# Kernel optimization log

Hardware: AMD Instinct MI355X
Metric: run time of the kernel (lower is better)

The kernel has to match this reference:

```python
import jax, jax.numpy as jnp
import numpy as np

N, IN_C, E = 50000, 512, 800000
H, C = 2, 64          # heads, per-head channels
HC = H * C            # 128
OUT_C = 2
B = 64                # number of graphs
EPS = 1e-5
NEG_SLOPE = 0.2


def gat_conv(x, src, dst, W, a_src, a_dst, bias):
    """PyG GATConv (concat=True, add_self_loops already included in src/dst)."""
    n = x.shape[0]
    h = (x @ W).reshape(n, H, C)                      # [N,H,C]
    alpha_src = (h * a_src[None]).sum(-1)             # [N,H]
    alpha_dst = (h * a_dst[None]).sum(-1)             # [N,H]
    e = jax.nn.leaky_relu(alpha_src[src] + alpha_dst[dst], NEG_SLOPE)  # [E,H]
    # segment softmax over incoming edges of each destination node
    m = jax.ops.segment_max(e, dst, num_segments=n)   # [N,H]
    ex = jnp.exp(e - m[dst])
    denom = jax.ops.segment_sum(ex, dst, num_segments=n)
    alpha = ex / denom[dst]                           # [E,H]
    msg = h[src] * alpha[:, :, None]                  # [E,H,C]
    out = jax.ops.segment_sum(msg, dst, num_segments=n)  # [N,H,C]
    return out.reshape(n, HC) + bias


def batch_norm(x, gamma, beta):
    # BatchNorm1d in training mode: batch statistics over the node dim
    mu = x.mean(0)
    var = x.var(0)
    return gamma * (x - mu) * jax.lax.rsqrt(var + EPS) + beta


def setup_inputs() -> dict:
    key = jax.random.key(0)
    ks = jax.random.split(key, 16)
    x = jax.random.normal(ks[0], (N, IN_C), dtype=jnp.float32)
    edge_index = jax.random.randint(ks[1], (2, E), 0, N, dtype=jnp.int64)
    batch = jnp.sort(jax.random.randint(ks[2], (N,), 0, B, dtype=jnp.int64))
    g = lambda k, sh, fan: jax.random.normal(k, sh, dtype=jnp.float32) * (1.0 / np.sqrt(fan))
    return {
        "x": x, "edge_index": edge_index, "batch": batch,
        "W1": g(ks[3], (IN_C, HC), IN_C),
        "att_src1": g(ks[4], (H, C), C), "att_dst1": g(ks[5], (H, C), C),
        "b1": jnp.zeros((HC,), jnp.float32),
        "gamma1": jnp.ones((HC,), jnp.float32), "beta1": jnp.zeros((HC,), jnp.float32),
        "W2": g(ks[6], (HC, HC), HC),
        "att_src2": g(ks[7], (H, C), C), "att_dst2": g(ks[8], (H, C), C),
        "b2": jnp.zeros((HC,), jnp.float32),
        "gamma2": jnp.ones((HC,), jnp.float32), "beta2": jnp.zeros((HC,), jnp.float32),
        "Wlin": g(ks[9], (HC, OUT_C), HC),
        "blin": jnp.zeros((OUT_C,), jnp.float32),
    }


def reference(x, edge_index, batch, W1, att_src1, att_dst1, b1, gamma1, beta1,
              W2, att_src2, att_dst2, b2, gamma2, beta2, Wlin, blin):
    n = x.shape[0]
    # GATConv adds self-loops by default
    loop = jnp.arange(n, dtype=edge_index.dtype)
    src = jnp.concatenate([edge_index[0], loop])
    dst = jnp.concatenate([edge_index[1], loop])

    h = gat_conv(x, src, dst, W1, att_src1, att_dst1, b1)
    h = jax.nn.relu(batch_norm(h, gamma1, beta1))
    h = gat_conv(h, src, dst, W2, att_src2, att_dst2, b2)
    h = jax.nn.relu(batch_norm(h, gamma2, beta2))

    # global mean pool over graphs
    sums = jax.ops.segment_sum(h, batch, num_segments=B)           # [B,HC]
    cnt = jax.ops.segment_sum(jnp.ones((n,), h.dtype), batch, num_segments=B)
    pooled = sums / jnp.maximum(cnt, 1.0)[:, None]
    return pooled @ Wlin + blin                                    # [B,OUT_C]
```

## Files before the change

### kernel.cpp

```cpp
#include <hip/hip_runtime.h>
#include <hip/hip_bf16.h>
#include <cstdint>
#include <cstddef>

#define NN      50000
#define IN_C    512
#define EE      800000
#define ETOT    850000
#define HH      2
#define CC      64
#define HC      128
#define BB      64
#define OUTC    2
#define NEG_SLOPE 0.2f
#define BN_EPS  1e-5f

#define NBLK_SCAN ((NN + 255) / 256)

typedef __bf16 bf16x8 __attribute__((ext_vector_type(8)));
typedef float  f32x4  __attribute__((ext_vector_type(4)));

__device__ __forceinline__ unsigned f2bf(float f) {
    __bf16 b = (__bf16)f;
    return (unsigned)__builtin_bit_cast(unsigned short, b);
}

__device__ __forceinline__ void edge_sd(const int* __restrict__ ei, int e, int& s, int& d) {
    if (e < EE) { s = ei[e]; d = ei[EE + e]; }
    else        { s = e - EE; d = e - EE; }
}

__global__ __launch_bounds__(256) void deg_kernel(const int* __restrict__ ei, int* __restrict__ deg)
{
    int e = blockIdx.x * 256 + threadIdx.x;
    if (e >= ETOT) return;
    int d = (e < EE) ? ei[EE + e] : (e - EE);
    atomicAdd(&deg[d], 1);
}

__global__ __launch_bounds__(256) void bsum_kernel(const int* __restrict__ deg, int* __restrict__ bsum)
{
    int i = blockIdx.x * 256 + threadIdx.x;
    int v = (i < NN) ? deg[i] : 0;
    int lane = threadIdx.x & 63, wv = threadIdx.x >> 6;
#pragma unroll
    for (int o = 32; o > 0; o >>= 1) v += __shfl_down(v, o);
    __shared__ int ws[4];
    if (lane == 0) ws[wv] = v;
    __syncthreads();
    if (threadIdx.x == 0) bsum[blockIdx.x] = ws[0] + ws[1] + ws[2] + ws[3];
}

__global__ __launch_bounds__(256) void bscan_kernel(
    const int* __restrict__ bsum, int* __restrict__ bofs, int* __restrict__ rowp)
{
    int t = threadIdx.x;
    int lane = t & 63, wv = t >> 6;
    int v = (t < NBLK_SCAN) ? bsum[t] : 0;
    int x = v;
#pragma unroll
    for (int o = 1; o < 64; o <<= 1) {
        int y = __shfl_up(x, o);
        if (lane >= o) x += y;
    }
    __shared__ int ws[4];
    if (lane == 63) ws[wv] = x;
    __syncthreads();
    int wo = 0;
#pragma unroll
    for (int w = 0; w < 4; ++w) if (w < wv) wo += ws[w];
    if (t < NBLK_SCAN) bofs[t] = x + wo - v;
    if (t == 0) rowp[NN] = ETOT;
}

__global__ __launch_bounds__(256) void bapply_kernel(
    const int* __restrict__ deg, const int* __restrict__ bofs,
    int* __restrict__ rowp, int* __restrict__ cur)
{
    int i = blockIdx.x * 256 + threadIdx.x;
    int v = (i < NN) ? deg[i] : 0;
    int lane = threadIdx.x & 63, wv = threadIdx.x >> 6;
    int x = v;
#pragma unroll
    for (int o = 1; o < 64; o <<= 1) {
        int y = __shfl_up(x, o);
        if (lane >= o) x += y;
    }
    __shared__ int ws[4];
    if (lane == 63) ws[wv] = x;
    __syncthreads();
    int wo = 0;
#pragma unroll
    for (int w = 0; w < 4; ++w) if (w < wv) wo += ws[w];
    if (i < NN) {
        int r = bofs[blockIdx.x] + x + wo - v;
        rowp[i] = r; cur[i] = r;
    }
}

__global__ __launch_bounds__(256) void scatter_kernel(
    const int* __restrict__ ei, int* __restrict__ cur, int* __restrict__ esrc)
{
    int e = blockIdx.x * 256 + threadIdx.x;
    if (e >= ETOT) return;
    int s, d; edge_sd(ei, e, s, d);
    int pos = atomicAdd(&cur[d], 1);
    esrc[pos] = s;
}

__global__ __launch_bounds__(256) void wfrag_kernel(
    const float* __restrict__ W, unsigned short* __restrict__ Wf, int K)
{
    int t = blockIdx.x * 256 + threadIdx.x;
    if (t >= K * 16) return;
    int lane = t & 63, frag = t >> 6;
    int kblk = frag >> 3, nt = frag & 7;
    int quad = lane >> 4, ln = lane & 15;
    int kbase = kblk * 32 + quad * 8;
    int n = nt * 16 + ln;
    unsigned short u[8];
#pragma unroll
    for (int j = 0; j < 8; ++j)
        u[j] = (unsigned short)f2bf(W[(size_t)(kbase + j) * HC + n]);
    ushort4 a; a.x = u[0]; a.y = u[1]; a.z = u[2]; a.w = u[3];
    ushort4 b; b.x = u[4]; b.y = u[5]; b.z = u[6]; b.w = u[7];
    *(ushort4*)(Wf + (size_t)t * 8)     = a;
    *(ushort4*)(Wf + (size_t)t * 8 + 4) = b;
}

template<int K, bool AFFINE>
__global__ __launch_bounds__(256, 3) void mfma_gemm_kernel(
    const float* __restrict__ A, const unsigned short* __restrict__ Wf,
    const float* __restrict__ atts, const float* __restrict__ attd,
    unsigned* __restrict__ hb, float* __restrict__ as_, float* __restrict__ ad_,
    const float* __restrict__ sc, const float* __restrict__ sh)
{
    constexpr int NSTEP = K >> 5;
    constexpr int AD = (NSTEP < 4) ? NSTEP : 4;

    const int tid  = threadIdx.x;
    const int wave = tid >> 6, lane = tid & 63;
    const int quad = lane >> 4, ln = lane & 15;
    const int m0 = blockIdx.x * 64;
    const int myrow = m0 + wave * 16 + ln;
    const bool rok = (myrow < NN);
    const float* arow = A + (size_t)(rok ? myrow : 0) * K + quad * 8;
    const unsigned short* wbase = Wf + lane * 8;

    f32x4 acc[8];
#pragma unroll
    for (int nt = 0; nt < 8; ++nt) acc[nt] = (f32x4){0.f, 0.f, 0.f, 0.f};

    const float4 z4 = make_float4(0.f, 0.f, 0.f, 0.f);
    float4 pa[AD], pb[AD];
#pragma unroll
    for (int d = 0; d < AD; ++d) {
        if (rok) {
            pa[d] = *(const float4*)(arow + d * 32);
            pb[d] = *(const float4*)(arow + d * 32 + 4);
        } else { pa[d] = z4; pb[d] = z4; }
    }

    bf16x8 bfr[2][8];
#pragma unroll
    for (int nt = 0; nt < 8; ++nt) bfr[0][nt] = *(const bf16x8*)(wbase + nt * 512);

#pragma unroll
    for (int ks = 0; ks < NSTEP; ++ks) {
        const int cur = ks & 1;
        if (ks + 1 < NSTEP) {
            const unsigned short* wfp = wbase + (size_t)(ks + 1) * 4096;
#pragma unroll
            for (int nt = 0; nt < 8; ++nt)
                bfr[cur ^ 1][nt] = *(const bf16x8*)(wfp + nt * 512);
        }

        float4 ca = pa[ks % AD], cb = pb[ks % AD];
        float va[8] = {ca.x, ca.y, ca.z, ca.w, cb.x, cb.y, cb.z, cb.w};
        if (AFFINE) {
            const int kk = ks * 32 + quad * 8;
            const float4 s0 = *(const float4*)(sc + kk), s1 = *(const float4*)(sc + kk + 4);
            const float4 h0 = *(const float4*)(sh + kk), h1 = *(const float4*)(sh + kk + 4);
            va[0] = fmaxf(fmaf(s0.x, va[0], h0.x), 0.f);
            va[1] = fmaxf(fmaf(s0.y, va[1], h0.y), 0.f);
            va[2] = fmaxf(fmaf(s0.z, va[2], h0.z), 0.f);
            va[3] = fmaxf(fmaf(s0.w, va[3], h0.w), 0.f);
            va[4] = fmaxf(fmaf(s1.x, va[4], h1.x), 0.f);
            va[5] = fmaxf(fmaf(s1.y, va[5], h1.y), 0.f);
            va[6] = fmaxf(fmaf(s1.z, va[6], h1.z), 0.f);
            va[7] = fmaxf(fmaf(s1.w, va[7], h1.w), 0.f);
        }
        union { bf16x8 v; unsigned short u[8]; } af;
#pragma unroll
        for (int j = 0; j < 8; ++j) af.u[j] = (unsigned short)f2bf(va[j]);

        if (ks + AD < NSTEP && rok) {
            const float* nx = arow + (size_t)(ks + AD) * 32;
            pa[ks % AD] = *(const float4*)nx;
            pb[ks % AD] = *(const float4*)(nx + 4);
        }

#pragma unroll
        for (int nt = 0; nt < 8; ++nt)
            acc[nt] = __builtin_amdgcn_mfma_f32_16x16x32_bf16(af.v, bfr[cur][nt], acc[nt], 0, 0, 0);
    }

    float wsv[8], wdv[8];
#pragma unroll
    for (int nt = 0; nt < 8; ++nt) { wsv[nt] = atts[nt * 16 + ln]; wdv[nt] = attd[nt * 16 + ln]; }

    const int mbase = m0 + wave * 16 + quad * 4;
#pragma unroll
    for (int r = 0; r < 4; ++r) {
        int m = mbase + r;
        bool ok = (m < NN);
        float ps0 = 0.f, ps1 = 0.f, pd0 = 0.f, pd1 = 0.f;
#pragma unroll
        for (int nt = 0; nt < 8; ++nt) {
            float v = acc[nt][r];
            if (nt < 4) { ps0 = fmaf(v, wsv[nt], ps0); pd0 = fmaf(v, wdv[nt], pd0); }
            else        { ps1 = fmaf(v, wsv[nt], ps1); pd1 = fmaf(v, wdv[nt], pd1); }
        }
#pragma unroll
        for (int nt = 0; nt < 4; ++nt) {
            unsigned pk = f2bf(acc[nt][r]) | (f2bf(acc[nt + 4][r]) << 16);
            if (ok) hb[(size_t)m * 64 + nt * 16 + ln] = pk;
        }
#pragma unroll
        for (int o = 8; o > 0; o >>= 1) {
            ps0 += __shfl_down(ps0, o); ps1 += __shfl_down(ps1, o);
            pd0 += __shfl_down(pd0, o); pd1 += __shfl_down(pd1, o);
        }
        if (ok && ln == 0) {
            *(float2*)&as_[m * 2] = make_float2(ps0, ps1);
            *(float2*)&ad_[m * 2] = make_float2(pd0, pd1);
        }
    }
}

__global__ __launch_bounds__(256) void gat_agg_kernel(
    const int* __restrict__ rowp, const int* __restrict__ esrc,
    const float* __restrict__ as_, const float* __restrict__ ad_,
    const unsigned* __restrict__ hb, float* __restrict__ out)
{
    int node = (blockIdx.x * 256 + threadIdx.x) >> 6;
    int lane = threadIdx.x & 63;
    if (node >= NN) return;
    int beg = rowp[node], end = rowp[node + 1];
    float2 adv = *(const float2*)&ad_[node * 2];

    float l0 = 0.f, l1 = 0.f, a0 = 0.f, a1 = 0.f;

    for (int j0 = beg; j0 < end; j0 += 64) {
        int nj = min(64, end - j0);
        int   sl  = 0;
        float p0l = 0.f, p1l = 0.f;
        if (j0 + lane < end) {
            sl = esrc[j0 + lane];
            float2 t = *(const float2*)&as_[sl * 2];
            float e0 = t.x + adv.x; e0 = fmaxf(e0, NEG_SLOPE * e0);
            float e1 = t.y + adv.y; e1 = fmaxf(e1, NEG_SLOPE * e1);
            p0l = __expf(e0); p1l = __expf(e1);
        }
        l0 += p0l; l1 += p1l;

        int j = 0;
        for (; j + 2 <= nj; j += 2) {
            int sA = __shfl(sl, j), sB = __shfl(sl, j + 1);
            unsigned uA = hb[(size_t)sA * 64 + lane];
            unsigned uB = hb[(size_t)sB * 64 + lane];
            float pA0 = __shfl(p0l, j),     pA1 = __shfl(p1l, j);
            float pB0 = __shfl(p0l, j + 1), pB1 = __shfl(p1l, j + 1);
            a0 = fmaf(pA0, __uint_as_float(uA << 16), a0);
            a1 = fmaf(pA1, __uint_as_float(uA & 0xffff0000u), a1);
            a0 = fmaf(pB0, __uint_as_float(uB << 16), a0);
            a1 = fmaf(pB1, __uint_as_float(uB & 0xffff0000u), a1);
        }
        if (j < nj) {
            int s = __shfl(sl, j);
            unsigned u = hb[(size_t)s * 64 + lane];
            float p0 = __shfl(p0l, j), p1 = __shfl(p1l, j);
            a0 = fmaf(p0, __uint_as_float(u << 16), a0);
            a1 = fmaf(p1, __uint_as_float(u & 0xffff0000u), a1);
        }
    }

#pragma unroll
    for (int o = 1; o < 64; o <<= 1) {
        l0 += __shfl_xor(l0, o); l1 += __shfl_xor(l1, o);
    }
    out[(size_t)node * HC + lane]      = a0 / l0;
    out[(size_t)node * HC + 64 + lane] = a1 / l1;
}

__global__ __launch_bounds__(256) void bn_stats_kernel(
    const float* __restrict__ x, float* __restrict__ stats)
{
    int c = threadIdx.x & 127;
    int half = threadIdx.x >> 7;
    float s = 0.f, sq = 0.f;
    for (int r = blockIdx.x * 2 + half; r < NN; r += gridDim.x * 2) {
        float v = x[(size_t)r * HC + c];
        s += v; sq += v * v;
    }
    __shared__ float ls[256], lq[256];
    ls[threadIdx.x] = s; lq[threadIdx.x] = sq;
    __syncthreads();
    if (half == 0) {
        s += ls[threadIdx.x + 128];
        sq += lq[threadIdx.x + 128];
        atomicAdd(&stats[c], s);
        atomicAdd(&stats[128 + c], sq);
    }
}

__global__ void bn_params_kernel(
    const float* __restrict__ stats, const float* __restrict__ gamma,
    const float* __restrict__ beta, float* __restrict__ sc, float* __restrict__ sh)
{
    int c = threadIdx.x;
    const float inv_n = 1.0f / (float)NN;
    float mu = stats[c] * inv_n;
    float var = stats[128 + c] * inv_n - mu * mu;
    float rs = rsqrtf(var + BN_EPS);
    float s = gamma[c] * rs;
    sc[c] = s;
    sh[c] = beta[c] - mu * s;
}

__global__ __launch_bounds__(256) void pool_kernel(
    const float* __restrict__ x, const float* __restrict__ sc,
    const float* __restrict__ sh, const int* __restrict__ batch,
    float* __restrict__ pool, float* __restrict__ cnt)
{
    int c = threadIdx.x & 127;
    int half = threadIdx.x >> 7;
    int r0 = blockIdx.x * 64;
    int rend = min(r0 + 64, NN);
    float s = sc[c], b = sh[c];
    int cur = -1; float acc = 0.f, ccount = 0.f;
    for (int r = r0 + half; r < rend; r += 2) {
        int g = batch[r];
        if (g != cur) {
            if (cur >= 0) {
                atomicAdd(&pool[cur * HC + c], acc);
                if (c == 0) atomicAdd(&cnt[cur], ccount);
            }
            cur = g; acc = 0.f; ccount = 0.f;
        }
        float v = x[(size_t)r * HC + c];
        acc += fmaxf(fmaf(s, v, b), 0.f);
        ccount += 1.f;
    }
    if (cur >= 0) {
        atomicAdd(&pool[cur * HC + c], acc);
        if (c == 0) atomicAdd(&cnt[cur], ccount);
    }
}

__global__ void final_kernel(
    const float* __restrict__ pool, const float* __restrict__ cnt,
    const float* __restrict__ Wlin, const float* __restrict__ blin,
    float* __restrict__ outp)
{
    int t = threadIdx.x;
    int b = t >> 1, oc = t & 1;
    float inv = 1.f / fmaxf(cnt[b], 1.f);
    float s = blin[oc];
    for (int c = 0; c < HC; ++c)
        s += pool[b * HC + c] * inv * Wlin[c * 2 + oc];
    outp[b * 2 + oc] = s;
}

static constexpr size_t OFF_OUT   = 0;
static constexpr size_t OFF_AS    = OFF_OUT + (size_t)NN*HC;
static constexpr size_t OFF_AD    = OFF_AS  + (size_t)NN*HH;
static constexpr size_t OFF_ST1   = OFF_AD  + (size_t)NN*HH;
static constexpr size_t OFF_ST2   = OFF_ST1 + 256;
static constexpr size_t OFF_SC1   = OFF_ST2 + 256;
static constexpr size_t OFF_SH1   = OFF_SC1 + 128;
static constexpr size_t OFF_SC2   = OFF_SH1 + 128;
static constexpr size_t OFF_SH2   = OFF_SC2 + 128;
static constexpr size_t OFF_POOL  = OFF_SH2 + 128;
static constexpr size_t OFF_CNT   = OFF_POOL+ (size_t)BB*HC;
static constexpr size_t OFF_ZEND  = OFF_CNT + BB;
static constexpr size_t IOFF_DEG  = 0;
static constexpr size_t IOFF_ROWP = IOFF_DEG  + NN;
static constexpr size_t IOFF_CUR  = IOFF_ROWP + NN + 1;
static constexpr size_t IOFF_BSUM = IOFF_CUR  + NN;
static constexpr size_t IOFF_BOFS = IOFF_BSUM + NBLK_SCAN;
static constexpr size_t IOFF_ESRC = IOFF_BOFS + NBLK_SCAN;
static constexpr size_t IOFF_HB   = (IOFF_ESRC + ETOT + 3) & ~(size_t)3;
static constexpr size_t IOFF_WF1  = IOFF_HB + (size_t)NN*64;
static constexpr size_t IOFF_WF2  = IOFF_WF1 + (size_t)IN_C*64;
static constexpr size_t IOFF_END  = IOFF_WF2 + (size_t)HC*64;

extern "C" void kernel_launch(void* const* d_in, const int* in_sizes, int n_in,
                              void* d_out, int out_size, void* d_ws, size_t ws_size,
                              hipStream_t stream)
{
    const float* x       = (const float*)d_in[0];
    const int*   ei      = (const int*)  d_in[1];
    const int*   batch   = (const int*)  d_in[2];
    const float* W1      = (const float*)d_in[3];
    const float* atts1   = (const float*)d_in[4];
    const float* attd1   = (const float*)d_in[5];
    const float* gamma1  = (const float*)d_in[7];
    const float* beta1   = (const float*)d_in[8];
    const float* W2      = (const float*)d_in[9];
    const float* atts2   = (const float*)d_in[10];
    const float* attd2   = (const float*)d_in[11];
    const float* gamma2  = (const float*)d_in[13];
    const float* beta2   = (const float*)d_in[14];
    const float* Wlin    = (const float*)d_in[15];
    const float* blin    = (const float*)d_in[16];
    float* outp = (float*)d_out;

    float* ws    = (float*)d_ws;
    float* out   = ws + OFF_OUT;
    float* as_   = ws + OFF_AS;
    float* ad_   = ws + OFF_AD;
    float* st1   = ws + OFF_ST1;
    float* st2   = ws + OFF_ST2;
    float* sc1   = ws + OFF_SC1;
    float* sh1   = ws + OFF_SH1;
    float* sc2   = ws + OFF_SC2;
    float* sh2   = ws + OFF_SH2;
    float* pool  = ws + OFF_POOL;
    float* cnt   = ws + OFF_CNT;

    int* iws  = (int*)(ws + OFF_ZEND);
    int* deg  = iws + IOFF_DEG;
    int* rowp = iws + IOFF_ROWP;
    int* curp = iws + IOFF_CUR;
    int* bsum = iws + IOFF_BSUM;
    int* bofs = iws + IOFF_BOFS;
    int* esrc = iws + IOFF_ESRC;
    unsigned* hb = (unsigned*)(iws + IOFF_HB);
    unsigned short* Wf1 = (unsigned short*)(iws + IOFF_WF1);
    unsigned short* Wf2 = (unsigned short*)(iws + IOFF_WF2);

    const int EDGE_BLK  = (ETOT + 255) / 256;
    const int GEMM_BLK  = (NN + 63) / 64;
    const int WAVE_BLK  = (NN + 3) / 4;
    const int POOL_BLK  = (NN + 63) / 64;

    hipMemsetAsync(st1, 0, (OFF_ZEND - OFF_ST1) * sizeof(float), stream);
    hipMemsetAsync(deg, 0, NN * sizeof(int), stream);

    wfrag_kernel<<<(IN_C * 16 + 255) / 256, 256, 0, stream>>>(W1, Wf1, IN_C);
    wfrag_kernel<<<(HC   * 16 + 255) / 256, 256, 0, stream>>>(W2, Wf2, HC);
    deg_kernel<<<EDGE_BLK, 256, 0, stream>>>(ei, deg);
    bsum_kernel<<<NBLK_SCAN, 256, 0, stream>>>(deg, bsum);
    bscan_kernel<<<1, 256, 0, stream>>>(bsum, bofs, rowp);
    bapply_kernel<<<NBLK_SCAN, 256, 0, stream>>>(deg, bofs, rowp, curp);
    scatter_kernel<<<EDGE_BLK, 256, 0, stream>>>(ei, curp, esrc);

    mfma_gemm_kernel<IN_C, false><<<GEMM_BLK, 256, 0, stream>>>(
        x, Wf1, atts1, attd1, hb, as_, ad_, nullptr, nullptr);
    gat_agg_kernel<<<WAVE_BLK, 256, 0, stream>>>(rowp, esrc, as_, ad_, hb, out);
    bn_stats_kernel<<<512, 256, 0, stream>>>(out, st1);
    bn_params_kernel<<<1, 128, 0, stream>>>(st1, gamma1, beta1, sc1, sh1);

    mfma_gemm_kernel<HC, true><<<GEMM_BLK, 256, 0, stream>>>(
        out, Wf2, atts2, attd2, hb, as_, ad_, sc1, sh1);
    gat_agg_kernel<<<WAVE_BLK, 256, 0, stream>>>(rowp, esrc, as_, ad_, hb, out);
    bn_stats_kernel<<<512, 256, 0, stream>>>(out, st2);
    bn_params_kernel<<<1, 128, 0, stream>>>(st2, gamma2, beta2, sc2, sh2);

    pool_kernel<<<POOL_BLK, 256, 0, stream>>>(out, sc2, sh2, batch, pool, cnt);
    final_kernel<<<1, 128, 0, stream>>>(pool, cnt, Wlin, blin, outp);
}
```

Before: 488.2 us.

## Partition CSR atomics by XCD, stage GEMM A tiles via LDS, unroll aggregation

The degree and scatter kernels now assign blocks to XCDs (blockIdx & 7). Each block scans a 2048-edge slot and only does atomics for destinations in its XCD's node range, so atomic traffic stays in one L2 but every edge is read eight times. The GEMM now loads A tiles through global_load_lds into a double-buffered, XOR-swizzled LDS buffer with a barrier per k-step, replacing register prefetch, and drops the occupancy hint. The aggregation inner loop is unrolled from 2 to 4 gathers per iteration to put more loads in flight.

```diff
diff --git a/kernel.cpp b/kernel.cpp
--- a/kernel.cpp
+++ b/kernel.cpp
@@ -17,6 +17,11 @@
 
 #define NBLK_SCAN ((NN + 255) / 256)
 
+#define NXCD     8
+#define NPX      ((NN + NXCD - 1) / NXCD)
+#define EDGES_PER_SLOT 2048
+#define NSLOT    ((ETOT + EDGES_PER_SLOT - 1) / EDGES_PER_SLOT)
+
 typedef __bf16 bf16x8 __attribute__((ext_vector_type(8)));
 typedef float  f32x4  __attribute__((ext_vector_type(4)));
 
@@ -25,17 +30,27 @@
     return (unsigned)__builtin_bit_cast(unsigned short, b);
 }
 
-__device__ __forceinline__ void edge_sd(const int* __restrict__ ei, int e, int& s, int& d) {
-    if (e < EE) { s = ei[e]; d = ei[EE + e]; }
-    else        { s = e - EE; d = e - EE; }
+__device__ __forceinline__ void gload_lds16(const float* g, float* l) {
+    __builtin_amdgcn_global_load_lds(
+        (const __attribute__((address_space(1))) unsigned*)g,
+        (__attribute__((address_space(3))) unsigned*)l,
+        16, 0, 0);
 }
 
 __global__ __launch_bounds__(256) void deg_kernel(const int* __restrict__ ei, int* __restrict__ deg)
 {
-    int e = blockIdx.x * 256 + threadIdx.x;
-    if (e >= ETOT) return;
-    int d = (e < EE) ? ei[EE + e] : (e - EE);
-    atomicAdd(&deg[d], 1);
+    const int xcd  = blockIdx.x & (NXCD - 1);
+    const int slot = blockIdx.x >> 3;
+    const int lo = xcd * NPX, hi = lo + NPX;
+    const int base = slot * EDGES_PER_SLOT;
+#pragma unroll
+    for (int it = 0; it < EDGES_PER_SLOT / 256; ++it) {
+        int e = base + it * 256 + threadIdx.x;
+        if (e < ETOT) {
+            int d = (e < EE) ? ei[EE + e] : (e - EE);
+            if (d >= lo && d < hi) atomicAdd(&deg[d], 1);
+        }
+    }
 }
 
 __global__ __launch_bounds__(256) void bsum_kernel(const int* __restrict__ deg, int* __restrict__ bsum)
@@ -101,11 +116,23 @@
 __global__ __launch_bounds__(256) void scatter_kernel(
     const int* __restrict__ ei, int* __restrict__ cur, int* __restrict__ esrc)
 {
-    int e = blockIdx.x * 256 + threadIdx.x;
-    if (e >= ETOT) return;
-    int s, d; edge_sd(ei, e, s, d);
-    int pos = atomicAdd(&cur[d], 1);
-    esrc[pos] = s;
+    const int xcd  = blockIdx.x & (NXCD - 1);
+    const int slot = blockIdx.x >> 3;
+    const int lo = xcd * NPX, hi = lo + NPX;
+    const int base = slot * EDGES_PER_SLOT;
+#pragma unroll
+    for (int it = 0; it < EDGES_PER_SLOT / 256; ++it) {
+        int e = base + it * 256 + threadIdx.x;
+        if (e < ETOT) {
+            int s, d;
+            if (e < EE) { s = ei[e]; d = ei[EE + e]; }
+            else        { s = e - EE; d = s; }
+            if (d >= lo && d < hi) {
+                int pos = atomicAdd(&cur[d], 1);
+                esrc[pos] = s;
+            }
+        }
+    }
 }
 
 __global__ __launch_bounds__(256) void wfrag_kernel(
@@ -129,38 +156,44 @@
 }
 
 template<int K, bool AFFINE>
-__global__ __launch_bounds__(256, 3) void mfma_gemm_kernel(
+__global__ __launch_bounds__(256) void mfma_gemm_kernel(
     const float* __restrict__ A, const unsigned short* __restrict__ Wf,
     const float* __restrict__ atts, const float* __restrict__ attd,
     unsigned* __restrict__ hb, float* __restrict__ as_, float* __restrict__ ad_,
     const float* __restrict__ sc, const float* __restrict__ sh)
 {
     constexpr int NSTEP = K >> 5;
-    constexpr int AD = (NSTEP < 4) ? NSTEP : 4;
+    __shared__ __align__(16) float Abuf[2][64 * 32];
 
     const int tid  = threadIdx.x;
     const int wave = tid >> 6, lane = tid & 63;
     const int quad = lane >> 4, ln = lane & 15;
     const int m0 = blockIdx.x * 64;
-    const int myrow = m0 + wave * 16 + ln;
-    const bool rok = (myrow < NN);
-    const float* arow = A + (size_t)(rok ? myrow : 0) * K + quad * 8;
+
+    const int srow = tid >> 3;
+    const int g    = (tid & 7) ^ (srow & 7);
+    int grow0 = m0 + srow;      if (grow0 > NN - 1) grow0 = NN - 1;
+    int grow1 = m0 + srow + 32; if (grow1 > NN - 1) grow1 = NN - 1;
+    const float* gsrc0 = A + (size_t)grow0 * K + g * 4;
+    const float* gsrc1 = A + (size_t)grow1 * K + g * 4;
+    float* ldst0 = &Abuf[0][wave * 256];
+    float* ldst1 = &Abuf[0][1024 + wave * 256];
+    const int bufstride = 64 * 32;
+
+    const int rr = wave * 16 + ln;
+    const int myrow = m0 + rr;
+    const int base_f = rr * 32;
+    const int sA = (((quad * 2)     ^ (rr & 7)) * 4);
+    const int sB = (((quad * 2 + 1) ^ (rr & 7)) * 4);
+
     const unsigned short* wbase = Wf + lane * 8;
 
     f32x4 acc[8];
 #pragma unroll
     for (int nt = 0; nt < 8; ++nt) acc[nt] = (f32x4){0.f, 0.f, 0.f, 0.f};
 
-    const float4 z4 = make_float4(0.f, 0.f, 0.f, 0.f);
-    float4 pa[AD], pb[AD];
-#pragma unroll
-    for (int d = 0; d < AD; ++d) {
-        if (rok) {
-            pa[d] = *(const float4*)(arow + d * 32);
-            pb[d] = *(const float4*)(arow + d * 32 + 4);
-        } else { pa[d] = z4; pb[d] = z4; }
-    }
-
+    gload_lds16(gsrc0, ldst0);
+    gload_lds16(gsrc1, ldst1);
     bf16x8 bfr[2][8];
 #pragma unroll
     for (int nt = 0; nt < 8; ++nt) bfr[0][nt] = *(const bf16x8*)(wbase + nt * 512);
@@ -168,15 +201,15 @@
 #pragma unroll
     for (int ks = 0; ks < NSTEP; ++ks) {
         const int cur = ks & 1;
+        __syncthreads();
         if (ks + 1 < NSTEP) {
-            const unsigned short* wfp = wbase + (size_t)(ks + 1) * 4096;
-#pragma unroll
-            for (int nt = 0; nt < 8; ++nt)
-                bfr[cur ^ 1][nt] = *(const bf16x8*)(wfp + nt * 512);
-        }
-
-        float4 ca = pa[ks % AD], cb = pb[ks % AD];
-        float va[8] = {ca.x, ca.y, ca.z, ca.w, cb.x, cb.y, cb.z, cb.w};
+            gload_lds16(gsrc0 + (size_t)(ks + 1) * 32, ldst0 + (cur ^ 1) * bufstride);
+            gload_lds16(gsrc1 + (size_t)(ks + 1) * 32, ldst1 + (cur ^ 1) * bufstride);
+        }
+
+        float4 fa = *(const float4*)&Abuf[cur][base_f + sA];
+        float4 fb = *(const float4*)&Abuf[cur][base_f + sB];
+        float va[8] = {fa.x, fa.y, fa.z, fa.w, fb.x, fb.y, fb.z, fb.w};
         if (AFFINE) {
             const int kk = ks * 32 + quad * 8;
             const float4 s0 = *(const float4*)(sc + kk), s1 = *(const float4*)(sc + kk + 4);
@@ -194,10 +227,11 @@
 #pragma unroll
         for (int j = 0; j < 8; ++j) af.u[j] = (unsigned short)f2bf(va[j]);
 
-        if (ks + AD < NSTEP && rok) {
-            const float* nx = arow + (size_t)(ks + AD) * 32;
-            pa[ks % AD] = *(const float4*)nx;
-            pb[ks % AD] = *(const float4*)(nx + 4);
+        if (ks + 1 < NSTEP) {
+            const unsigned short* wfp = wbase + (size_t)(ks + 1) * 4096;
+#pragma unroll
+            for (int nt = 0; nt < 8; ++nt)
+                bfr[cur ^ 1][nt] = *(const bf16x8*)(wfp + nt * 512);
         }
 
 #pragma unroll
@@ -265,18 +299,27 @@
         l0 += p0l; l1 += p1l;
 
         int j = 0;
-        for (; j + 2 <= nj; j += 2) {
-            int sA = __shfl(sl, j), sB = __shfl(sl, j + 1);
+        for (; j + 4 <= nj; j += 4) {
+            int sA = __shfl(sl, j),     sB = __shfl(sl, j + 1);
+            int sC = __shfl(sl, j + 2), sD = __shfl(sl, j + 3);
             unsigned uA = hb[(size_t)sA * 64 + lane];
             unsigned uB = hb[(size_t)sB * 64 + lane];
+            unsigned uC = hb[(size_t)sC * 64 + lane];
+            unsigned uD = hb[(size_t)sD * 64 + lane];
             float pA0 = __shfl(p0l, j),     pA1 = __shfl(p1l, j);
             float pB0 = __shfl(p0l, j + 1), pB1 = __shfl(p1l, j + 1);
+            float pC0 = __shfl(p0l, j + 2), pC1 = __shfl(p1l, j + 2);
+            float pD0 = __shfl(p0l, j + 3), pD1 = __shfl(p1l, j + 3);
             a0 = fmaf(pA0, __uint_as_float(uA << 16), a0);
             a1 = fmaf(pA1, __uint_as_float(uA & 0xffff0000u), a1);
             a0 = fmaf(pB0, __uint_as_float(uB << 16), a0);
             a1 = fmaf(pB1, __uint_as_float(uB & 0xffff0000u), a1);
-        }
-        if (j < nj) {
+            a0 = fmaf(pC0, __uint_as_float(uC << 16), a0);
+            a1 = fmaf(pC1, __uint_as_float(uC & 0xffff0000u), a1);
+            a0 = fmaf(pD0, __uint_as_float(uD << 16), a0);
+            a1 = fmaf(pD1, __uint_as_float(uD & 0xffff0000u), a1);
+        }
+        for (; j < nj; ++j) {
             int s = __shfl(sl, j);
             unsigned u = hb[(size_t)s * 64 + lane];
             float p0 = __shfl(p0l, j), p1 = __shfl(p1l, j);
@@ -440,7 +483,7 @@
     unsigned short* Wf1 = (unsigned short*)(iws + IOFF_WF1);
     unsigned short* Wf2 = (unsigned short*)(iws + IOFF_WF2);
 
-    const int EDGE_BLK  = (ETOT + 255) / 256;
+    const int BIN_BLK   = NXCD * NSLOT;
     const int GEMM_BLK  = (NN + 63) / 64;
     const int WAVE_BLK  = (NN + 3) / 4;
     const int POOL_BLK  = (NN + 63) / 64;
@@ -450,11 +493,11 @@
 
     wfrag_kernel<<<(IN_C * 16 + 255) / 256, 256, 0, stream>>>(W1, Wf1, IN_C);
     wfrag_kernel<<<(HC   * 16 + 255) / 256, 256, 0, stream>>>(W2, Wf2, HC);
-    deg_kernel<<<EDGE_BLK, 256, 0, stream>>>(ei, deg);
+    deg_kernel<<<BIN_BLK, 256, 0, stream>>>(ei, deg);
     bsum_kernel<<<NBLK_SCAN, 256, 0, stream>>>(deg, bsum);
     bscan_kernel<<<1, 256, 0, stream>>>(bsum, bofs, rowp);
     bapply_kernel<<<NBLK_SCAN, 256, 0, stream>>>(deg, bofs, rowp, curp);
-    scatter_kernel<<<EDGE_BLK, 256, 0, stream>>>(ei, curp, esrc);
+    scatter_kernel<<<BIN_BLK, 256, 0, stream>>>(ei, curp, esrc);
 
     mfma_gemm_kernel<IN_C, false><<<GEMM_BLK, 256, 0, stream>>>(
         x, Wf1, atts1, attd1, hb, as_, ad_, nullptr, nullptr);
```

After: 469.1 us. 1.04x faster.
